# Performance work log

Measured on AMD Instinct MI355X. Metric: run time of the kernel, lower is better.

Reference implementation:

```python
import jax, jax.numpy as jnp
import numpy as np

B, H, S, D = 4, 8, 8192, 64


def setup_inputs() -> dict:
    key = jax.random.key(0)
    kq, kk, kv_, kqm, kkm = jax.random.split(key, 5)
    q = jax.random.normal(kq, (B, H, S, D), dtype=jnp.float32)
    k = jax.random.normal(kk, (B, H, S, D), dtype=jnp.float32)
    v = jax.random.normal(kv_, (B, H, S, D), dtype=jnp.float32)
    q_mask = jax.random.randint(kqm, (B, S), 0, 2).astype(jnp.bool_)
    kv_mask = jax.random.randint(kkm, (B, S), 0, 2).astype(jnp.bool_)
    return {"q": q, "k": k, "v": v, "q_mask": q_mask, "kv_mask": kv_mask}


def reference(q, k, v, q_mask, kv_mask):
    # Linear (kernelized) attention branch: feature map phi(x) = elu(x) + 1
    qe = jax.nn.elu(q) + 1.0
    ke = jax.nn.elu(k) + 1.0
    qm = q_mask.astype(q.dtype)[:, None, :, None]   # [B,1,S,1]
    km = kv_mask.astype(q.dtype)[:, None, :, None]
    qe = qe * qm
    ke = ke * km
    ve = v * km
    s = v.shape[2]
    # kv: [B,H,D,D] contraction over kv sequence
    kv = jnp.einsum('bhsd,bhsc->bhdc', ke, ve / s)
    # normalizer per query position: [B,H,L]
    div = 1.0 / (jnp.einsum('bhld,bhsd->bhl', qe, ke) + 1e-6)
    out = s * jnp.einsum('bhld,bhdc,bhl->bhlc', qe, kv, div)
    return out
```

## Files before the change

### kernel.cpp

```cpp
#include <hip/hip_runtime.h>
#include <hip/hip_bf16.h>


#define S_LEN 8192
#define NBH 32
#define DIM 64
#define KVSTRIDE (64*64 + 64)
#define MAXCHUNK 32

__device__ __forceinline__ float elu1(float x) {
  return x > 0.0f ? (x + 1.0f) : __expf(x);
}

__global__ __launch_bounds__(256) void k1_partial(
    const float* __restrict__ kin, const float* __restrict__ vin,
    const int* __restrict__ kv_mask, float* __restrict__ partials, int seg_rows) {
  __shared__ float ke_s[64][64];
  __shared__ float ve_s[64][64];
  const int tid = threadIdx.x;
  const int seg = blockIdx.x, bh = blockIdx.y, b = bh >> 3;
  const int dg = tid >> 4, cg = tid & 15;
  float acc[4][4] = {};
  float ks[4] = {};
  const int rbase = seg * seg_rows;

  for (int t0 = 0; t0 < seg_rows; t0 += 64) {
    const int r0 = rbase + t0;
    const float4* kp = (const float4*)(kin + ((size_t)bh * S_LEN + r0) * DIM);
    const float4* vp = (const float4*)(vin + ((size_t)bh * S_LEN + r0) * DIM);
#pragma unroll
    for (int i = 0; i < 4; ++i) {
      int qd = i * 256 + tid;
      int sl = qd >> 4, d = (qd & 15) * 4;
      float m = kv_mask[b * S_LEN + r0 + sl] ? 1.0f : 0.0f;
      float4 kw = kp[qd];
      float4 vw = vp[qd];
      float4 kf, vf;
      kf.x = elu1(kw.x) * m;
      kf.y = elu1(kw.y) * m;
      kf.z = elu1(kw.z) * m;
      kf.w = elu1(kw.w) * m;
      float mv = m * (1.0f / 8192.0f);
      vf.x = vw.x * mv;
      vf.y = vw.y * mv;
      vf.z = vw.z * mv;
      vf.w = vw.w * mv;
      *(float4*)&ke_s[sl][d] = kf;
      *(float4*)&ve_s[sl][d] = vf;
    }
    __syncthreads();
#pragma unroll 4
    for (int s = 0; s < 64; ++s) {
      float4 kd = *(const float4*)&ke_s[s][dg * 4];
      float4 vq = *(const float4*)&ve_s[s][cg * 4];
      float ka[4] = {kd.x, kd.y, kd.z, kd.w};
      float va[4] = {vq.x, vq.y, vq.z, vq.w};
#pragma unroll
      for (int i2 = 0; i2 < 4; ++i2) {
        ks[i2] += ka[i2];
#pragma unroll
        for (int j = 0; j < 4; ++j) acc[i2][j] += ka[i2] * va[j];
      }
    }
    __syncthreads();
  }

  float* p = partials + ((size_t)bh * gridDim.x + seg) * KVSTRIDE;
#pragma unroll
  for (int i2 = 0; i2 < 4; ++i2)
#pragma unroll
    for (int j = 0; j < 4; ++j)
      p[(dg * 4 + i2) * 64 + cg * 4 + j] = acc[i2][j];
  if (cg == 0) {
#pragma unroll
    for (int i2 = 0; i2 < 4; ++i2) p[4096 + dg * 4 + i2] = ks[i2];
  }
}

__global__ __launch_bounds__(256) void k2_reduce(const float* __restrict__ partials,
                                                 float* __restrict__ kvfinal, int nchunk) {
  const int idx = blockIdx.x * 256 + threadIdx.x;
  if (idx >= NBH * KVSTRIDE) return;
  const int bh = idx / KVSTRIDE;
  const int e  = idx - bh * KVSTRIDE;
  const float* p = partials + (size_t)bh * nchunk * KVSTRIDE + e;
  float s0 = 0.f, s1 = 0.f, s2 = 0.f, s3 = 0.f;
  int c = 0;
  for (; c + 4 <= nchunk; c += 4) {
    s0 += p[(size_t)(c + 0) * KVSTRIDE];
    s1 += p[(size_t)(c + 1) * KVSTRIDE];
    s2 += p[(size_t)(c + 2) * KVSTRIDE];
    s3 += p[(size_t)(c + 3) * KVSTRIDE];
  }
  for (; c < nchunk; ++c) s0 += p[(size_t)c * KVSTRIDE];
  kvfinal[(size_t)bh * KVSTRIDE + e] = (s0 + s1) + (s2 + s3);
}

__global__ __launch_bounds__(256) void k3_out(
    const float* __restrict__ qin, const int* __restrict__ q_mask,
    const float* __restrict__ kvfinal, float* __restrict__ out) {
  __shared__ float kv_s[64][64];
  __shared__ float ksum_s[64];
  __shared__ float qeT[64][68];
  const int tid = threadIdx.x;
  const int rb = blockIdx.x, bh = blockIdx.y, b = bh >> 3;
  const int r0 = rb * 64;
  const float* kvp = kvfinal + (size_t)bh * KVSTRIDE;
#pragma unroll
  for (int i = 0; i < 16; ++i) {
    int idx = i * 256 + tid;
    kv_s[idx >> 6][idx & 63] = kvp[idx];
  }
  if (tid < 64) ksum_s[tid] = kvp[4096 + tid];
  const float4* qp = (const float4*)(qin + ((size_t)bh * S_LEN + r0) * DIM);
#pragma unroll
  for (int i = 0; i < 4; ++i) {
    int qd = i * 256 + tid;
    int rl = qd >> 4, d = (qd & 15) * 4;
    float m = q_mask[b * S_LEN + r0 + rl] ? 1.0f : 0.0f;
    float4 qw = qp[qd];
    qeT[d][rl]     = elu1(qw.x) * m;
    qeT[d + 1][rl] = elu1(qw.y) * m;
    qeT[d + 2][rl] = elu1(qw.z) * m;
    qeT[d + 3][rl] = elu1(qw.w) * m;
  }
  __syncthreads();
  const int rg = tid >> 4, cg = tid & 15;
  float acc[4][4] = {};
  float den[4] = {};
#pragma unroll 4
  for (int d = 0; d < 64; ++d) {
    float4 qv  = *(const float4*)&qeT[d][rg * 4];
    float4 kvv = *(const float4*)&kv_s[d][cg * 4];
    float ksd = ksum_s[d];
    float qa[4] = {qv.x, qv.y, qv.z, qv.w};
    float ca[4] = {kvv.x, kvv.y, kvv.z, kvv.w};
#pragma unroll
    for (int i2 = 0; i2 < 4; ++i2) {
      den[i2] += qa[i2] * ksd;
#pragma unroll
      for (int j = 0; j < 4; ++j) acc[i2][j] += qa[i2] * ca[j];
    }
  }
#pragma unroll
  for (int i2 = 0; i2 < 4; ++i2) {
    int r = r0 + rg * 4 + i2;
    float inv = 8192.0f / (den[i2] + 1e-6f);
    float4 o;
    o.x = acc[i2][0] * inv;
    o.y = acc[i2][1] * inv;
    o.z = acc[i2][2] * inv;
    o.w = acc[i2][3] * inv;
    *(float4*)(out + ((size_t)bh * S_LEN + r) * DIM + cg * 4) = o;
  }
}

extern "C" void kernel_launch(void* const* d_in, const int* in_sizes, int n_in,
                              void* d_out, int out_size, void* d_ws, size_t ws_size,
                              hipStream_t stream) {
  const float* q = (const float*)d_in[0];
  const float* k = (const float*)d_in[1];
  const float* v = (const float*)d_in[2];
  const int* qm = (const int*)d_in[3];
  const int* km = (const int*)d_in[4];
  float* out = (float*)d_out;

  int nchunk = MAXCHUNK;
  while (nchunk > 1 &&
         ((size_t)NBH * (nchunk + 1) * KVSTRIDE * sizeof(float)) > ws_size)
    nchunk >>= 1;
  float* partials = (float*)d_ws;
  float* kvfinal  = partials + (size_t)NBH * nchunk * KVSTRIDE;
  int seg_rows = S_LEN / nchunk;

  k1_partial<<<dim3(nchunk, NBH), 256, 0, stream>>>(k, v, km, partials, seg_rows);
  int n_elem = NBH * KVSTRIDE;
  k2_reduce<<<dim3((n_elem + 255) / 256), 256, 0, stream>>>(partials, kvfinal, nchunk);
  k3_out<<<dim3(S_LEN / 64, NBH), 256, 0, stream>>>(q, qm, kvfinal, out);
}
```

Before: 247.9 us.

## Use bf16x3 split MFMA for kv accumulation and output projection

Replaces the scalar FP32 FMA inner loops in the kv-partial and output kernels with 16x16x32 bf16 MFMA instructions. Each operand is split into high and low bf16 parts, and three MFMAs per product approximate FP32 accuracy. The k-sum and the normalizer are also computed with MFMA, the former against a vector of ones. The reduce kernel now writes kv transposed and pre-split into bf16 hi/lo buffers for the output kernel. The kernels are memory-bound, so compute savings may matter little, and the split adds conversion work, transposed shared-memory stores and some precision risk.

```diff
diff --git a/kernel.cpp b/kernel.cpp
--- a/kernel.cpp
+++ b/kernel.cpp
@@ -4,85 +4,121 @@
 
 #define S_LEN 8192
 #define NBH 32
-#define DIM 64
-#define KVSTRIDE (64*64 + 64)
-#define MAXCHUNK 32
+#define KVSTRIDE 4160
+
+typedef __attribute__((ext_vector_type(8))) short short8;
+typedef __attribute__((ext_vector_type(4))) float f32x4;
 
 __device__ __forceinline__ float elu1(float x) {
   return x > 0.0f ? (x + 1.0f) : __expf(x);
 }
+__device__ __forceinline__ unsigned short f2bf(float x) {
+  __hip_bfloat16 h = __float2bfloat16(x);
+  union { __hip_bfloat16 b; unsigned short u; } cv; cv.b = h; return cv.u;
+}
+__device__ __forceinline__ float bf2f(unsigned short u) {
+  return __uint_as_float(((unsigned)u) << 16);
+}
+__device__ __forceinline__ void split2(float x, unsigned short& hi, unsigned short& lo) {
+  hi = f2bf(x);
+  lo = f2bf(x - bf2f(hi));
+}
+__device__ __forceinline__ short8 ones8() {
+  short8 o;
+#pragma unroll
+  for (int i = 0; i < 8; ++i) o[i] = (short)0x3F80;
+  return o;
+}
+
+#define MFMA(a,b,c) __builtin_amdgcn_mfma_f32_16x16x32_bf16((a),(b),(c),0,0,0)
 
 __global__ __launch_bounds__(256) void k1_partial(
     const float* __restrict__ kin, const float* __restrict__ vin,
     const int* __restrict__ kv_mask, float* __restrict__ partials, int seg_rows) {
-  __shared__ float ke_s[64][64];
-  __shared__ float ve_s[64][64];
+  __shared__ unsigned short keT_h[64 * 72];
+  __shared__ unsigned short keT_l[64 * 72];
+  __shared__ unsigned short veT_h[64 * 72];
+  __shared__ unsigned short veT_l[64 * 72];
   const int tid = threadIdx.x;
   const int seg = blockIdx.x, bh = blockIdx.y, b = bh >> 3;
-  const int dg = tid >> 4, cg = tid & 15;
-  float acc[4][4] = {};
-  float ks[4] = {};
+  const int dp = tid & 31;
+  const int so = tid >> 5;
+  const int lane = tid & 63, w = tid >> 6;
+  const int mrow = lane & 15, qd4 = lane >> 4;
+  const short8 one = ones8();
+
+  f32x4 acc[4]; f32x4 accs;
+#pragma unroll
+  for (int t = 0; t < 4; ++t) acc[t] = (f32x4){0.f, 0.f, 0.f, 0.f};
+  accs = (f32x4){0.f, 0.f, 0.f, 0.f};
+
   const int rbase = seg * seg_rows;
-
   for (int t0 = 0; t0 < seg_rows; t0 += 64) {
     const int r0 = rbase + t0;
-    const float4* kp = (const float4*)(kin + ((size_t)bh * S_LEN + r0) * DIM);
-    const float4* vp = (const float4*)(vin + ((size_t)bh * S_LEN + r0) * DIM);
-#pragma unroll
-    for (int i = 0; i < 4; ++i) {
-      int qd = i * 256 + tid;
-      int sl = qd >> 4, d = (qd & 15) * 4;
-      float m = kv_mask[b * S_LEN + r0 + sl] ? 1.0f : 0.0f;
-      float4 kw = kp[qd];
-      float4 vw = vp[qd];
-      float4 kf, vf;
-      kf.x = elu1(kw.x) * m;
-      kf.y = elu1(kw.y) * m;
-      kf.z = elu1(kw.z) * m;
-      kf.w = elu1(kw.w) * m;
+    const float* kp = kin + ((size_t)bh * S_LEN + r0 + so * 8) * 64 + dp * 2;
+    const float* vp = vin + ((size_t)bh * S_LEN + r0 + so * 8) * 64 + dp * 2;
+    union { unsigned short u[8]; uint4 v; } kh0, kh1, kl0, kl1, vh0, vh1, vl0, vl1;
+#pragma unroll
+    for (int r = 0; r < 8; ++r) {
+      float m = kv_mask[b * S_LEN + r0 + so * 8 + r] ? 1.0f : 0.0f;
+      float2 kw = *(const float2*)(kp + (size_t)r * 64);
+      float2 vw = *(const float2*)(vp + (size_t)r * 64);
+      float ka = elu1(kw.x) * m;
+      float kb = elu1(kw.y) * m;
       float mv = m * (1.0f / 8192.0f);
-      vf.x = vw.x * mv;
-      vf.y = vw.y * mv;
-      vf.z = vw.z * mv;
-      vf.w = vw.w * mv;
-      *(float4*)&ke_s[sl][d] = kf;
-      *(float4*)&ve_s[sl][d] = vf;
+      float va = vw.x * mv, vb = vw.y * mv;
+      split2(ka, kh0.u[r], kl0.u[r]);
+      split2(kb, kh1.u[r], kl1.u[r]);
+      split2(va, vh0.u[r], vl0.u[r]);
+      split2(vb, vh1.u[r], vl1.u[r]);
     }
+    const int d0 = dp * 2;
+    *(uint4*)&keT_h[(d0    ) * 72 + so * 8] = kh0.v;
+    *(uint4*)&keT_h[(d0 + 1) * 72 + so * 8] = kh1.v;
+    *(uint4*)&keT_l[(d0    ) * 72 + so * 8] = kl0.v;
+    *(uint4*)&keT_l[(d0 + 1) * 72 + so * 8] = kl1.v;
+    *(uint4*)&veT_h[(d0    ) * 72 + so * 8] = vh0.v;
+    *(uint4*)&veT_h[(d0 + 1) * 72 + so * 8] = vh1.v;
+    *(uint4*)&veT_l[(d0    ) * 72 + so * 8] = vl0.v;
+    *(uint4*)&veT_l[(d0 + 1) * 72 + so * 8] = vl1.v;
     __syncthreads();
-#pragma unroll 4
-    for (int s = 0; s < 64; ++s) {
-      float4 kd = *(const float4*)&ke_s[s][dg * 4];
-      float4 vq = *(const float4*)&ve_s[s][cg * 4];
-      float ka[4] = {kd.x, kd.y, kd.z, kd.w};
-      float va[4] = {vq.x, vq.y, vq.z, vq.w};
-#pragma unroll
-      for (int i2 = 0; i2 < 4; ++i2) {
-        ks[i2] += ka[i2];
-#pragma unroll
-        for (int j = 0; j < 4; ++j) acc[i2][j] += ka[i2] * va[j];
+#pragma unroll
+    for (int k0 = 0; k0 < 64; k0 += 32) {
+      short8 a_h = *(const short8*)&keT_h[(w * 16 + mrow) * 72 + k0 + qd4 * 8];
+      short8 a_l = *(const short8*)&keT_l[(w * 16 + mrow) * 72 + k0 + qd4 * 8];
+      accs = MFMA(a_h, one, accs);
+      accs = MFMA(a_l, one, accs);
+#pragma unroll
+      for (int t = 0; t < 4; ++t) {
+        short8 b_h = *(const short8*)&veT_h[(t * 16 + mrow) * 72 + k0 + qd4 * 8];
+        short8 b_l = *(const short8*)&veT_l[(t * 16 + mrow) * 72 + k0 + qd4 * 8];
+        acc[t] = MFMA(a_h, b_h, acc[t]);
+        acc[t] = MFMA(a_h, b_l, acc[t]);
+        acc[t] = MFMA(a_l, b_h, acc[t]);
       }
     }
     __syncthreads();
   }
-
   float* p = partials + ((size_t)bh * gridDim.x + seg) * KVSTRIDE;
 #pragma unroll
-  for (int i2 = 0; i2 < 4; ++i2)
-#pragma unroll
-    for (int j = 0; j < 4; ++j)
-      p[(dg * 4 + i2) * 64 + cg * 4 + j] = acc[i2][j];
-  if (cg == 0) {
-#pragma unroll
-    for (int i2 = 0; i2 < 4; ++i2) p[4096 + dg * 4 + i2] = ks[i2];
-  }
-}
-
-__global__ __launch_bounds__(256) void k2_reduce(const float* __restrict__ partials,
-                                                 float* __restrict__ kvfinal, int nchunk) {
+  for (int t = 0; t < 4; ++t)
+#pragma unroll
+    for (int r = 0; r < 4; ++r)
+      p[(w * 16 + qd4 * 4 + r) * 64 + t * 16 + mrow] = acc[t][r];
+  if (mrow == 0) {
+#pragma unroll
+    for (int r = 0; r < 4; ++r) p[4096 + w * 16 + qd4 * 4 + r] = accs[r];
+  }
+}
+
+__global__ __launch_bounds__(256) void k2_reduce(
+    const float* __restrict__ partials,
+    unsigned short* __restrict__ kvTh, unsigned short* __restrict__ kvTl,
+    unsigned short* __restrict__ ksh, unsigned short* __restrict__ ksl, int nchunk) {
   const int idx = blockIdx.x * 256 + threadIdx.x;
   if (idx >= NBH * KVSTRIDE) return;
   const int bh = idx / KVSTRIDE;
-  const int e  = idx - bh * KVSTRIDE;
+  const int e = idx - bh * KVSTRIDE;
   const float* p = partials + (size_t)bh * nchunk * KVSTRIDE + e;
   float s0 = 0.f, s1 = 0.f, s2 = 0.f, s3 = 0.f;
   int c = 0;
@@ -93,65 +129,90 @@
     s3 += p[(size_t)(c + 3) * KVSTRIDE];
   }
   for (; c < nchunk; ++c) s0 += p[(size_t)c * KVSTRIDE];
-  kvfinal[(size_t)bh * KVSTRIDE + e] = (s0 + s1) + (s2 + s3);
+  float s = (s0 + s1) + (s2 + s3);
+  unsigned short hi, lo;
+  split2(s, hi, lo);
+  if (e < 4096) {
+    int d = e >> 6, cc = e & 63;
+    kvTh[(size_t)bh * 4096 + cc * 64 + d] = hi;
+    kvTl[(size_t)bh * 4096 + cc * 64 + d] = lo;
+  } else {
+    int d = e - 4096;
+    ksh[bh * 64 + d] = hi;
+    ksl[bh * 64 + d] = lo;
+  }
 }
 
 __global__ __launch_bounds__(256) void k3_out(
     const float* __restrict__ qin, const int* __restrict__ q_mask,
-    const float* __restrict__ kvfinal, float* __restrict__ out) {
-  __shared__ float kv_s[64][64];
-  __shared__ float ksum_s[64];
-  __shared__ float qeT[64][68];
+    const unsigned short* __restrict__ kvTh_g, const unsigned short* __restrict__ kvTl_g,
+    const unsigned short* __restrict__ ksh_g, const unsigned short* __restrict__ ksl_g,
+    float* __restrict__ out) {
+  __shared__ unsigned short qe_h[64 * 72];
+  __shared__ unsigned short qe_l[64 * 72];
+  __shared__ unsigned short kv_h[64 * 72];
+  __shared__ unsigned short kv_l[64 * 72];
+  __shared__ __align__(16) unsigned short ks_h[64];
+  __shared__ __align__(16) unsigned short ks_l[64];
   const int tid = threadIdx.x;
   const int rb = blockIdx.x, bh = blockIdx.y, b = bh >> 3;
   const int r0 = rb * 64;
-  const float* kvp = kvfinal + (size_t)bh * KVSTRIDE;
-#pragma unroll
-  for (int i = 0; i < 16; ++i) {
-    int idx = i * 256 + tid;
-    kv_s[idx >> 6][idx & 63] = kvp[idx];
-  }
-  if (tid < 64) ksum_s[tid] = kvp[4096 + tid];
-  const float4* qp = (const float4*)(qin + ((size_t)bh * S_LEN + r0) * DIM);
 #pragma unroll
   for (int i = 0; i < 4; ++i) {
     int qd = i * 256 + tid;
-    int rl = qd >> 4, d = (qd & 15) * 4;
-    float m = q_mask[b * S_LEN + r0 + rl] ? 1.0f : 0.0f;
-    float4 qw = qp[qd];
-    qeT[d][rl]     = elu1(qw.x) * m;
-    qeT[d + 1][rl] = elu1(qw.y) * m;
-    qeT[d + 2][rl] = elu1(qw.z) * m;
-    qeT[d + 3][rl] = elu1(qw.w) * m;
+    int l = qd >> 4, dq = qd & 15;
+    float m = q_mask[b * S_LEN + r0 + l] ? 1.0f : 0.0f;
+    float4 qw = *(const float4*)(qin + ((size_t)bh * S_LEN + r0 + l) * 64 + dq * 4);
+    union { unsigned short u[4]; uint2 v; } h, lo;
+    float e0 = elu1(qw.x) * m, e1 = elu1(qw.y) * m, e2 = elu1(qw.z) * m, e3 = elu1(qw.w) * m;
+    split2(e0, h.u[0], lo.u[0]);
+    split2(e1, h.u[1], lo.u[1]);
+    split2(e2, h.u[2], lo.u[2]);
+    split2(e3, h.u[3], lo.u[3]);
+    *(uint2*)&qe_h[l * 72 + dq * 4] = h.v;
+    *(uint2*)&qe_l[l * 72 + dq * 4] = lo.v;
+  }
+  for (int e = tid; e < 2048; e += 256) {
+    int c = (e * 2) >> 6, d = (e * 2) & 63;
+    *(unsigned*)&kv_h[c * 72 + d] = *(const unsigned*)(kvTh_g + (size_t)bh * 4096 + e * 2);
+    *(unsigned*)&kv_l[c * 72 + d] = *(const unsigned*)(kvTl_g + (size_t)bh * 4096 + e * 2);
+  }
+  if (tid < 64) {
+    ks_h[tid] = ksh_g[bh * 64 + tid];
+    ks_l[tid] = ksl_g[bh * 64 + tid];
   }
   __syncthreads();
-  const int rg = tid >> 4, cg = tid & 15;
-  float acc[4][4] = {};
-  float den[4] = {};
-#pragma unroll 4
-  for (int d = 0; d < 64; ++d) {
-    float4 qv  = *(const float4*)&qeT[d][rg * 4];
-    float4 kvv = *(const float4*)&kv_s[d][cg * 4];
-    float ksd = ksum_s[d];
-    float qa[4] = {qv.x, qv.y, qv.z, qv.w};
-    float ca[4] = {kvv.x, kvv.y, kvv.z, kvv.w};
-#pragma unroll
-    for (int i2 = 0; i2 < 4; ++i2) {
-      den[i2] += qa[i2] * ksd;
-#pragma unroll
-      for (int j = 0; j < 4; ++j) acc[i2][j] += qa[i2] * ca[j];
+  const int lane = tid & 63, w = tid >> 6;
+  const int mrow = lane & 15, qd4 = lane >> 4;
+  f32x4 acc[4]; f32x4 accd;
+#pragma unroll
+  for (int t = 0; t < 4; ++t) acc[t] = (f32x4){0.f, 0.f, 0.f, 0.f};
+  accd = (f32x4){0.f, 0.f, 0.f, 0.f};
+#pragma unroll
+  for (int k0 = 0; k0 < 64; k0 += 32) {
+    short8 a_h = *(const short8*)&qe_h[(w * 16 + mrow) * 72 + k0 + qd4 * 8];
+    short8 a_l = *(const short8*)&qe_l[(w * 16 + mrow) * 72 + k0 + qd4 * 8];
+    short8 s_h = *(const short8*)&ks_h[k0 + qd4 * 8];
+    short8 s_l = *(const short8*)&ks_l[k0 + qd4 * 8];
+    accd = MFMA(a_h, s_h, accd);
+    accd = MFMA(a_h, s_l, accd);
+    accd = MFMA(a_l, s_h, accd);
+#pragma unroll
+    for (int t = 0; t < 4; ++t) {
+      short8 b_h = *(const short8*)&kv_h[(t * 16 + mrow) * 72 + k0 + qd4 * 8];
+      short8 b_l = *(const short8*)&kv_l[(t * 16 + mrow) * 72 + k0 + qd4 * 8];
+      acc[t] = MFMA(a_h, b_h, acc[t]);
+      acc[t] = MFMA(a_h, b_l, acc[t]);
+      acc[t] = MFMA(a_l, b_h, acc[t]);
     }
   }
 #pragma unroll
-  for (int i2 = 0; i2 < 4; ++i2) {
-    int r = r0 + rg * 4 + i2;
-    float inv = 8192.0f / (den[i2] + 1e-6f);
-    float4 o;
-    o.x = acc[i2][0] * inv;
-    o.y = acc[i2][1] * inv;
-    o.z = acc[i2][2] * inv;
-    o.w = acc[i2][3] * inv;
-    *(float4*)(out + ((size_t)bh * S_LEN + r) * DIM + cg * 4) = o;
+  for (int r = 0; r < 4; ++r) {
+    float inv = 8192.0f / (accd[r] + 1e-6f);
+    int row = r0 + w * 16 + qd4 * 4 + r;
+#pragma unroll
+    for (int t = 0; t < 4; ++t)
+      out[((size_t)bh * S_LEN + row) * 64 + t * 16 + mrow] = acc[t][r] * inv;
   }
 }
 
@@ -165,16 +226,22 @@
   const int* km = (const int*)d_in[4];
   float* out = (float*)d_out;
 
-  int nchunk = MAXCHUNK;
-  while (nchunk > 1 &&
-         ((size_t)NBH * (nchunk + 1) * KVSTRIDE * sizeof(float)) > ws_size)
+  int nchunk = 32;
+  while (nchunk > 1) {
+    size_t need = (size_t)NBH * nchunk * KVSTRIDE * 4
+                + (size_t)NBH * 4096 * 2 * 2 + (size_t)NBH * 64 * 2 * 2;
+    if (need <= ws_size) break;
     nchunk >>= 1;
+  }
   float* partials = (float*)d_ws;
-  float* kvfinal  = partials + (size_t)NBH * nchunk * KVSTRIDE;
+  unsigned short* kvTh = (unsigned short*)(partials + (size_t)NBH * nchunk * KVSTRIDE);
+  unsigned short* kvTl = kvTh + (size_t)NBH * 4096;
+  unsigned short* ksh  = kvTl + (size_t)NBH * 4096;
+  unsigned short* ksl  = ksh + NBH * 64;
   int seg_rows = S_LEN / nchunk;
 
   k1_partial<<<dim3(nchunk, NBH), 256, 0, stream>>>(k, v, km, partials, seg_rows);
   int n_elem = NBH * KVSTRIDE;
-  k2_reduce<<<dim3((n_elem + 255) / 256), 256, 0, stream>>>(partials, kvfinal, nchunk);
-  k3_out<<<dim3(S_LEN / 64, NBH), 256, 0, stream>>>(q, qm, kvfinal, out);
-}
+  k2_reduce<<<dim3((n_elem + 255) / 256), 256, 0, stream>>>(partials, kvTh, kvTl, ksh, ksl, nchunk);
+  k3_out<<<dim3(S_LEN / 64, NBH), 256, 0, stream>>>(q, qm, kvTh, kvTl, ksh, ksl, out);
+}
```

New measurement: 238.5 us. 1.04x faster.
